# Performance work log

Hardware: AMD Instinct MI355X
Metric: run time of the kernel (lower is better)

The kernel has to match this reference:

```python
import jax, jax.numpy as jnp
import numpy as np

CHUNK = 2048  # mirrors torch.chunk(pc, len(pc)//2048) with N a multiple of 2048


def _half(src, ref):
    """Faithful to the original: for each chunk of `src`, compute the
    [M, chunk] squared-distance matrix against `ref` and take min over the
    chunk axis (dim 1), yielding an M-vector per chunk; concatenate.
    Result shape: [num_chunks * M]."""
    chunks = src.reshape(-1, CHUNK, src.shape[-1])  # [num_chunks, CHUNK, 3]

    def per_chunk(chunk):
        diff = ref[:, None, :] - chunk[None, :, :]          # [M, CHUNK, 3]
        d = jnp.square(jnp.sqrt(jnp.sum(diff * diff, -1)))  # norm(...)**2
        return jnp.min(d, axis=1)                           # [M]

    return jax.lax.map(per_chunk, chunks).reshape(-1)


def setup_inputs() -> dict:
    key = jax.random.key(0)
    k1, k2 = jax.random.split(key)
    output_pc = jax.random.normal(k1, (1, 16384, 3), dtype=jnp.float32)
    gt_pc = jax.random.normal(k2, (1, 16384, 3), dtype=jnp.float32)
    return {"output_pc": output_pc, "gt_pc": gt_pc}


def reference(output_pc, gt_pc):
    pc1 = jnp.squeeze(output_pc)  # [N, 3]
    pc2 = jnp.squeeze(gt_pc)      # [M, 3]
    dist1 = _half(pc1, pc2)       # [ (N//CHUNK) * M ]
    dist2 = _half(pc2, pc1)       # [ (M//CHUNK) * N ]
    return jnp.mean(dist1) + jnp.mean(dist2)
```

## Files before the change

kernel.cpp:

```cpp
#include <hip/hip_runtime.h>
#include <float.h>

#define CHUNK 2048
#define SUB   512
#define MBLK  128

typedef __attribute__((ext_vector_type(8)))  short short8;
typedef __attribute__((ext_vector_type(16))) float f32x16;

static __device__ __forceinline__ unsigned short f2bf(float f) {
    unsigned u = __float_as_uint(f);
    return (unsigned short)((u + 0x7FFFu + ((u >> 16) & 1u)) >> 16);
}
static __device__ __forceinline__ float bf2f(unsigned short s) {
    return __uint_as_float(((unsigned)s) << 16);
}

__global__ void pack_kernel(const float* __restrict__ p1,
                            const float* __restrict__ p2, int n1, int n2,
                            unsigned short* __restrict__ Arec,
                            unsigned short* __restrict__ Brec,
                            unsigned* __restrict__ U, int utotal)
{
    int i = blockIdx.x * blockDim.x + threadIdx.x;
    int nthreads = gridDim.x * blockDim.x;
    for (int idx = i; idx < utotal; idx += nthreads) U[idx] = 0x7F800000u;

    if (i >= n1 + n2) return;
    const bool isA = (i < n1);
    const float* s = isA ? p1 : p2;
    const int j = isA ? i : i - n1;
    float x = s[3 * j + 0], y = s[3 * j + 1], z = s[3 * j + 2];

    unsigned short r[16];
    if (isA) {
        unsigned short hx = f2bf(x), hy = f2bf(y), hz = f2bf(z);
        unsigned short lx = f2bf(x - bf2f(hx)), ly = f2bf(y - bf2f(hy)),
                       lz = f2bf(z - bf2f(hz));
        float sp = fmaf(x, x, fmaf(y, y, z * z));
        unsigned short sh = f2bf(sp), sl = f2bf(sp - bf2f(sh));
        r[0]=hx; r[1]=hy; r[2]=hz;  r[3]=lx; r[4]=ly; r[5]=lz;
        r[6]=hx; r[7]=hy; r[8]=hz;  r[9]=lx; r[10]=ly; r[11]=lz;
        r[12]=sh; r[13]=sl; r[14]=0x3F80; r[15]=0x3F80;
        unsigned short* dst = Arec + (size_t)j * 16;
#pragma unroll
        for (int t = 0; t < 16; ++t) dst[t] = r[t];
    } else {
        float ux = -2.0f * x, uy = -2.0f * y, uz = -2.0f * z;
        unsigned short hx = f2bf(ux), hy = f2bf(uy), hz = f2bf(uz);
        unsigned short lx = f2bf(ux - bf2f(hx)), ly = f2bf(uy - bf2f(hy)),
                       lz = f2bf(uz - bf2f(hz));
        float sq = fmaf(x, x, fmaf(y, y, z * z));
        unsigned short sh = f2bf(sq), sl = f2bf(sq - bf2f(sh));
        r[0]=hx; r[1]=hy; r[2]=hz;  r[3]=hx; r[4]=hy; r[5]=hz;
        r[6]=lx; r[7]=ly; r[8]=lz;  r[9]=lx; r[10]=ly; r[11]=lz;
        r[12]=0x3F80; r[13]=0x3F80; r[14]=sh; r[15]=sl;
        unsigned short* dst = Brec + (size_t)j * 16;
#pragma unroll
        for (int t = 0; t < 16; ++t) dst[t] = r[t];
    }
}

__global__ __launch_bounds__(256, 8)
void chamfer_mfma(const unsigned short* __restrict__ Arec,
                  const unsigned short* __restrict__ Brec,
                  unsigned* __restrict__ colU, unsigned* __restrict__ rowU,
                  int n1, int n2)
{
    __shared__ float colminW[4 * SUB];

    const int tid  = threadIdx.x;
    const int g    = blockIdx.x;
    const int yb   = blockIdx.y;
    const int lane = tid & 63;
    const int w    = tid >> 6;
    const int half = lane >> 5;
    const int l31  = lane & 31;

    const int colbase = yb * SUB;
    const int cc      = yb >> 2;
    const int c1      = g >> 4;

    const int rA = g * MBLK + w * 32 + l31;
    short8 aA = *(const short8*)(Arec + (size_t)rA * 16 + half * 8);

    const unsigned short* bp =
        Brec + (size_t)(colbase + l31) * 16 + half * 8;

    const f32x16 z16 = {0,0,0,0, 0,0,0,0, 0,0,0,0, 0,0,0,0};
    float rm[16];
#pragma unroll
    for (int r = 0; r < 16; ++r) rm[r] = FLT_MAX;

#pragma unroll 2
    for (int t = 0; t < SUB / 32; ++t) {
        short8 b = *(const short8*)(bp + (size_t)t * 512);
        f32x16 d = __builtin_amdgcn_mfma_f32_32x32x16_bf16(aA, b, z16, 0, 0, 0);
#pragma unroll
        for (int r = 0; r < 16; ++r) rm[r] = fminf(rm[r], d[r]);
        float c01 = fminf(fminf(d[0], d[1]),  fminf(d[2], d[3]));
        float c23 = fminf(fminf(d[4], d[5]),  fminf(d[6], d[7]));
        float c45 = fminf(fminf(d[8], d[9]),  fminf(d[10], d[11]));
        float c67 = fminf(fminf(d[12], d[13]), fminf(d[14], d[15]));
        float cm  = fminf(fminf(c01, c23), fminf(c45, c67));
        cm = fminf(cm, __shfl_xor(cm, 32));
        cm = fmaxf(cm, 0.0f);
        if (half == 0) colminW[w * SUB + t * 32 + l31] = cm;
    }

#pragma unroll
    for (int r = 0; r < 8; ++r) {
        float lo = fminf(rm[r],     __shfl_xor(rm[r],     16));
        float hi = fminf(rm[r + 8], __shfl_xor(rm[r + 8], 16));
        rm[r] = (l31 & 16) ? hi : lo;
    }
#pragma unroll
    for (int r = 0; r < 4; ++r) {
        float lo = fminf(rm[r],     __shfl_xor(rm[r],     8));
        float hi = fminf(rm[r + 4], __shfl_xor(rm[r + 4], 8));
        rm[r] = (l31 & 8) ? hi : lo;
    }
#pragma unroll
    for (int r = 0; r < 2; ++r) {
        float lo = fminf(rm[r],     __shfl_xor(rm[r],     4));
        float hi = fminf(rm[r + 2], __shfl_xor(rm[r + 2], 4));
        rm[r] = (l31 & 4) ? hi : lo;
    }
    {
        float lo = fminf(rm[0], __shfl_xor(rm[0], 2));
        float hi = fminf(rm[1], __shfl_xor(rm[1], 2));
        rm[0] = (l31 & 2) ? hi : lo;
    }
    float v = fminf(rm[0], __shfl_xor(rm[0], 1));
    if ((l31 & 1) == 0) {
        int r = (l31 >> 1) & 15;
        int rowl = (r & 3) + 8 * (r >> 2) + 4 * half;
        int grow = g * MBLK + w * 32 + rowl;
        atomicMin(&rowU[(size_t)cc * n1 + grow],
                  __float_as_uint(fmaxf(v, 0.0f)));
    }

    __syncthreads();
    for (int cb = tid; cb < SUB; cb += 256) {
        float m = fminf(fminf(colminW[0 * SUB + cb], colminW[1 * SUB + cb]),
                        fminf(colminW[2 * SUB + cb], colminW[3 * SUB + cb]));
        atomicMin(&colU[(size_t)c1 * n2 + colbase + cb], __float_as_uint(m));
    }
}

__global__ __launch_bounds__(256)
void pass2_kernel(const unsigned* __restrict__ U, float* __restrict__ out,
                  int total1, int total2, float s1, float s2)
{
    __shared__ float wred[4];
    const int n = total1 + total2;
    float s = 0.0f;
    for (int i = blockIdx.x * 256 + threadIdx.x; i < n; i += gridDim.x * 256) {
        float v = __uint_as_float(U[i]);
        s += v * (i < total1 ? s1 : s2);
    }
#pragma unroll
    for (int off = 32; off > 0; off >>= 1) s += __shfl_down(s, off);
    const int lane = threadIdx.x & 63, w = threadIdx.x >> 6;
    if (lane == 0) wred[w] = s;
    __syncthreads();
    if (threadIdx.x == 0)
        atomicAdd(out, wred[0] + wred[1] + wred[2] + wred[3]);
}

#define FB_RPT  2
#define FB_TILE (256 * FB_RPT)
__global__ __launch_bounds__(256, 2)
void chamfer_valu(const float* __restrict__ p1, const float* __restrict__ p2,
                  int n1, int n2, float* __restrict__ out)
{
    __shared__ float4 q[CHUNK];
    __shared__ float wsum[4];
    const int dir = blockIdx.z;
    const float* __restrict__ src = dir ? p2 : p1;
    const float* __restrict__ ref = dir ? p1 : p2;
    const int nsrc = dir ? n2 : n1;
    const int m    = dir ? n1 : n2;
    const int nchunks = nsrc / CHUNK;
    const int c = blockIdx.y;
    const int tile0 = blockIdx.x * FB_TILE;
    if (c >= nchunks || tile0 >= m) return;
    const float scale = 1.0f / ((float)nchunks * (float)m);
    const float* __restrict__ chunk = src + (size_t)c * CHUNK * 3;
    for (int k = threadIdx.x; k < CHUNK; k += 256) {
        float x = chunk[3*k], y = chunk[3*k+1], z = chunk[3*k+2];
        q[k] = make_float4(x, y, z, fmaf(x, x, fmaf(y, y, z * z)));
    }
    __syncthreads();
    float px[FB_RPT], py[FB_RPT], pz[FB_RPT], sp[FB_RPT], mna[FB_RPT], mnb[FB_RPT];
    bool valid[FB_RPT];
#pragma unroll
    for (int r = 0; r < FB_RPT; ++r) {
        int j = tile0 + threadIdx.x + r * 256;
        valid[r] = (j < m);
        int jj = valid[r] ? j : 0;
        float x = ref[3*jj], y = ref[3*jj+1], z = ref[3*jj+2];
        px[r] = -2.0f*x; py[r] = -2.0f*y; pz[r] = -2.0f*z;
        sp[r] = fmaf(x, x, fmaf(y, y, z * z));
        mna[r] = FLT_MAX; mnb[r] = FLT_MAX;
    }
#pragma unroll 2
    for (int k = 0; k < CHUNK; k += 2) {
        float4 qa = q[k], qb = q[k+1];
#pragma unroll
        for (int r = 0; r < FB_RPT; ++r) {
            mna[r] = fminf(mna[r], fmaf(px[r], qa.x, fmaf(py[r], qa.y, fmaf(pz[r], qa.z, qa.w))));
            mnb[r] = fminf(mnb[r], fmaf(px[r], qb.x, fmaf(py[r], qb.y, fmaf(pz[r], qb.z, qb.w))));
        }
    }
    float sum = 0.0f;
#pragma unroll
    for (int r = 0; r < FB_RPT; ++r)
        if (valid[r]) sum += fmaxf(fminf(mna[r], mnb[r]) + sp[r], 0.0f);
#pragma unroll
    for (int off = 32; off > 0; off >>= 1) sum += __shfl_down(sum, off);
    if ((threadIdx.x & 63) == 0) wsum[threadIdx.x >> 6] = sum;
    __syncthreads();
    if (threadIdx.x == 0)
        atomicAdd(out, (wsum[0]+wsum[1]+wsum[2]+wsum[3]) * scale);
}

extern "C" void kernel_launch(void* const* d_in, const int* in_sizes, int n_in,
                              void* d_out, int out_size, void* d_ws, size_t ws_size,
                              hipStream_t stream)
{
    const float* p1 = (const float*)d_in[0];
    const float* p2 = (const float*)d_in[1];
    float* out = (float*)d_out;
    const int n1 = in_sizes[0] / 3;
    const int n2 = in_sizes[1] / 3;

    const int nc1 = n1 / CHUNK, nc2 = n2 / CHUNK;
    unsigned short* Arec = (unsigned short*)d_ws;
    unsigned short* Brec = Arec + (size_t)n1 * 16;
    unsigned* U   = (unsigned*)(Brec + (size_t)n2 * 16);
    const int total1 = nc1 * n2;
    const int total2 = nc2 * n1;
    unsigned* colU = U;
    unsigned* rowU = U + total1;
    const size_t need = (size_t)n1 * 32 + (size_t)n2 * 32 +
                        (size_t)(total1 + total2) * 4;

    const bool shapes_ok = (n1 % CHUNK == 0) && (n2 % CHUNK == 0) &&
                           (n1 % MBLK == 0) && (n2 % SUB == 0);

    if (shapes_ok && ws_size >= need) {
        pack_kernel<<<(n1 + n2 + 255) / 256, 256, 0, stream>>>(
            p1, p2, n1, n2, Arec, Brec, U, total1 + total2);
        dim3 grid(n1 / MBLK, n2 / SUB);
        chamfer_mfma<<<grid, 256, 0, stream>>>(Arec, Brec, colU, rowU, n1, n2);
        pass2_kernel<<<256, 256, 0, stream>>>(
            U, out, total1, total2,
            1.0f / ((float)nc1 * (float)n2), 1.0f / ((float)nc2 * (float)n1));
    } else {
        const int t1 = (n2 + FB_TILE - 1) / FB_TILE;
        const int t2 = (n1 + FB_TILE - 1) / FB_TILE;
        dim3 grid(max(t1, t2), max(nc1, nc2), 2);
        chamfer_valu<<<grid, 256, 0, stream>>>(p1, p2, n1, n2, out);
    }
}
```

Before: 94.01 us.

## Replace global atomicMin reductions with partial-min buffers reduced in pass2

Result: slower. 96.25 us (+2.4%).

```diff
diff --git a/kernel.cpp b/kernel.cpp
--- a/kernel.cpp
+++ b/kernel.cpp
@@ -19,13 +19,9 @@
 __global__ void pack_kernel(const float* __restrict__ p1,
                             const float* __restrict__ p2, int n1, int n2,
                             unsigned short* __restrict__ Arec,
-                            unsigned short* __restrict__ Brec,
-                            unsigned* __restrict__ U, int utotal)
+                            unsigned short* __restrict__ Brec)
 {
     int i = blockIdx.x * blockDim.x + threadIdx.x;
-    int nthreads = gridDim.x * blockDim.x;
-    for (int idx = i; idx < utotal; idx += nthreads) U[idx] = 0x7F800000u;
-
     if (i >= n1 + n2) return;
     const bool isA = (i < n1);
     const float* s = isA ? p1 : p2;
@@ -61,10 +57,10 @@
     }
 }
 
-__global__ __launch_bounds__(256, 8)
+__global__ __launch_bounds__(256, 4)
 void chamfer_mfma(const unsigned short* __restrict__ Arec,
                   const unsigned short* __restrict__ Brec,
-                  unsigned* __restrict__ colU, unsigned* __restrict__ rowU,
+                  float* __restrict__ colpart, float* __restrict__ rowpart,
                   int n1, int n2)
 {
     __shared__ float colminW[4 * SUB];
@@ -78,8 +74,6 @@
     const int l31  = lane & 31;
 
     const int colbase = yb * SUB;
-    const int cc      = yb >> 2;
-    const int c1      = g >> 4;
 
     const int rA = g * MBLK + w * 32 + l31;
     short8 aA = *(const short8*)(Arec + (size_t)rA * 16 + half * 8);
@@ -136,28 +130,44 @@
         int r = (l31 >> 1) & 15;
         int rowl = (r & 3) + 8 * (r >> 2) + 4 * half;
         int grow = g * MBLK + w * 32 + rowl;
-        atomicMin(&rowU[(size_t)cc * n1 + grow],
-                  __float_as_uint(fmaxf(v, 0.0f)));
+        rowpart[(size_t)yb * n1 + grow] = fmaxf(v, 0.0f);
     }
 
     __syncthreads();
     for (int cb = tid; cb < SUB; cb += 256) {
         float m = fminf(fminf(colminW[0 * SUB + cb], colminW[1 * SUB + cb]),
                         fminf(colminW[2 * SUB + cb], colminW[3 * SUB + cb]));
-        atomicMin(&colU[(size_t)c1 * n2 + colbase + cb], __float_as_uint(m));
+        colpart[(size_t)g * n2 + colbase + cb] = m;
     }
 }
 
 __global__ __launch_bounds__(256)
-void pass2_kernel(const unsigned* __restrict__ U, float* __restrict__ out,
-                  int total1, int total2, float s1, float s2)
+void pass2_kernel(const float* __restrict__ colpart,
+                  const float* __restrict__ rowpart, float* __restrict__ out,
+                  int n1, int n2, int total1, int total2, float s1, float s2)
 {
     __shared__ float wred[4];
     const int n = total1 + total2;
     float s = 0.0f;
-    for (int i = blockIdx.x * 256 + threadIdx.x; i < n; i += gridDim.x * 256) {
-        float v = __uint_as_float(U[i]);
-        s += v * (i < total1 ? s1 : s2);
+    for (int idx = blockIdx.x * 256 + threadIdx.x; idx < n;
+         idx += gridDim.x * 256) {
+        float m = FLT_MAX;
+        if (idx < total1) {
+            int c1  = idx / n2;
+            int col = idx - c1 * n2;
+#pragma unroll
+            for (int t = 0; t < CHUNK / MBLK; ++t)
+                m = fminf(m, colpart[(size_t)(c1 * (CHUNK / MBLK) + t) * n2 + col]);
+            s += fmaxf(m, 0.0f) * s1;
+        } else {
+            int i2  = idx - total1;
+            int cc  = i2 / n1;
+            int row = i2 - cc * n1;
+#pragma unroll
+            for (int t = 0; t < CHUNK / SUB; ++t)
+                m = fminf(m, rowpart[(size_t)(cc * (CHUNK / SUB) + t) * n1 + row]);
+            s += fmaxf(m, 0.0f) * s2;
+        }
     }
 #pragma unroll
     for (int off = 32; off > 0; off >>= 1) s += __shfl_down(s, off);
@@ -236,26 +246,27 @@
     const int n2 = in_sizes[1] / 3;
 
     const int nc1 = n1 / CHUNK, nc2 = n2 / CHUNK;
+    const int ng  = n1 / MBLK;
+    const int nyb = n2 / SUB;
+
     unsigned short* Arec = (unsigned short*)d_ws;
     unsigned short* Brec = Arec + (size_t)n1 * 16;
-    unsigned* U   = (unsigned*)(Brec + (size_t)n2 * 16);
-    const int total1 = nc1 * n2;
-    const int total2 = nc2 * n1;
-    unsigned* colU = U;
-    unsigned* rowU = U + total1;
+    float* colpart = (float*)(Brec + (size_t)n2 * 16);
+    float* rowpart = colpart + (size_t)ng * n2;
     const size_t need = (size_t)n1 * 32 + (size_t)n2 * 32 +
-                        (size_t)(total1 + total2) * 4;
+                        ((size_t)ng * n2 + (size_t)nyb * n1) * 4;
 
     const bool shapes_ok = (n1 % CHUNK == 0) && (n2 % CHUNK == 0) &&
                            (n1 % MBLK == 0) && (n2 % SUB == 0);
 
     if (shapes_ok && ws_size >= need) {
         pack_kernel<<<(n1 + n2 + 255) / 256, 256, 0, stream>>>(
-            p1, p2, n1, n2, Arec, Brec, U, total1 + total2);
-        dim3 grid(n1 / MBLK, n2 / SUB);
-        chamfer_mfma<<<grid, 256, 0, stream>>>(Arec, Brec, colU, rowU, n1, n2);
-        pass2_kernel<<<256, 256, 0, stream>>>(
-            U, out, total1, total2,
+            p1, p2, n1, n2, Arec, Brec);
+        dim3 grid(ng, nyb);
+        chamfer_mfma<<<grid, 256, 0, stream>>>(Arec, Brec, colpart, rowpart, n1, n2);
+        const int total1 = nc1 * n2, total2 = nc2 * n1;
+        pass2_kernel<<<512, 256, 0, stream>>>(
+            colpart, rowpart, out, n1, n2, total1, total2,
             1.0f / ((float)nc1 * (float)n2), 1.0f / ((float)nc2 * (float)n1));
     } else {
         const int t1 = (n2 + FB_TILE - 1) / FB_TILE;
```
